# Kernel tuning notes

Hardware: AMD Instinct MI355X
Metric: run time of the kernel (lower is better)

The kernel has to match this reference:

```python
import jax, jax.numpy as jnp
import numpy as np

COUPLE_STRENGTH = 0.1
ITER_FISTA = 16
ITER_EIGENVAL = 20


def setup_inputs() -> dict:
    key = jax.random.key(0)
    k1, k2 = jax.random.split(key)
    # light field patches: (b, N, u, v, s, t, ch)
    x = jax.random.normal(k1, (8, 256, 5, 5, 4, 4, 3), dtype=jnp.float32)
    dim_signal = 5 * 5 * 4 * 4 * 3  # 1200
    dim_dict = 2 * dim_signal       # overcompleteness = 2 -> 2400
    D = jax.random.normal(k2, (dim_signal, dim_dict), dtype=jnp.float32)
    D = D / jnp.linalg.norm(D, axis=0, keepdims=True)  # UnitNorm(axis=0) constraint
    return {"x": x, "dictionary": D}


def _max_eigval(D):
    """von Mises power iteration for largest eigenvalue of D^T D."""
    v0 = jax.random.normal(jax.random.key(42), (D.shape[1],), dtype=D.dtype)
    v0 = v0 / jnp.linalg.norm(v0)

    def step(v, _):
        w = D.T @ (D @ v)
        n = jnp.linalg.norm(w)
        return w / n, n

    _, norms = jax.lax.scan(step, v0, None, length=ITER_EIGENVAL)
    return norms[-1]


def _soft_threshold(x, thr):
    return jnp.sign(x) * jnp.maximum(jnp.abs(x) - thr, 0.0)


def _sparse_code_fista(x2, D):
    """x2: (B, N, dim_signal); D: (dim_signal, dim_dict) -> codes (B, N, dim_dict)."""
    L = _max_eigval(D)            # Lipschitz constant of grad of 0.5*||Dz - x||^2
    thr = COUPLE_STRENGTH / L
    z0 = jnp.zeros(x2.shape[:-1] + (D.shape[1],), dtype=x2.dtype)
    carry0 = (z0, z0, jnp.float32(1.0))  # (z, y, t)

    def step(carry, _):
        z, y, t = carry
        recon = jnp.einsum('bnk,dk->bnd', y, D)             # (B,N,ds)
        grad = jnp.einsum('bnd,dk->bnk', recon - x2, D)     # (B,N,dd)
        z_new = _soft_threshold(y - grad / L, thr)
        t_new = 0.5 * (1.0 + jnp.sqrt(1.0 + 4.0 * t * t))
        y_new = z_new + ((t - 1.0) / t_new) * (z_new - z)   # Nesterov momentum
        return (z_new, y_new, t_new), None

    (z, _, _), _ = jax.lax.scan(step, carry0, None, length=ITER_FISTA)
    return z


def reference(x, dictionary):
    B, N, u, v, s, t, ch = x.shape
    x2 = x.reshape(B, N, u * v * s * t * ch)
    code = jax.lax.stop_gradient(_sparse_code_fista(x2, dictionary))
    recon = jnp.einsum('bnk,dk->bnd', code, dictionary)  # matmul(x, D, transpose_b=True)
    return recon.reshape(B, N, u, v, s, t, ch)
```

## Files before the change

kernel.cpp:

```cpp
#include <hip/hip_runtime.h>
#include <hip/hip_bf16.h>
#include <cmath>

#define DS 1200
#define DD 2400
#define MR 2048
#define KP 1216
#define NP1 1280
#define NG 2432
#define PPI 150

typedef __attribute__((ext_vector_type(8))) short s16x8;
typedef __attribute__((ext_vector_type(4))) float f32x4;

__device__ __forceinline__ float s2f(short s) {
    union { unsigned u; float f; } c;
    c.u = ((unsigned)(unsigned short)s) << 16;
    return c.f;
}
__device__ __forceinline__ short f2s(float f) {
    __hip_bfloat16 h = __float2bfloat16(f);
    return *reinterpret_cast<short*>(&h);
}


__device__ __forceinline__ unsigned rotl32(unsigned x, int d) {
    return (x << d) | (x >> (32 - d));
}

__device__ void threefry2x32(unsigned k0, unsigned k1, unsigned x0, unsigned x1,
                             unsigned* o0, unsigned* o1) {
    unsigned ks0 = k0, ks1 = k1, ks2 = k0 ^ k1 ^ 0x1BD11BDAu;
    const int rotA[4] = {13, 15, 26, 6};
    const int rotB[4] = {17, 29, 16, 24};
    x0 += ks0; x1 += ks1;
    #pragma unroll
    for (int r = 0; r < 4; r++) { x0 += x1; x1 = rotl32(x1, rotA[r]); x1 ^= x0; }
    x0 += ks1; x1 += ks2 + 1u;
    #pragma unroll
    for (int r = 0; r < 4; r++) { x0 += x1; x1 = rotl32(x1, rotB[r]); x1 ^= x0; }
    x0 += ks2; x1 += ks0 + 2u;
    #pragma unroll
    for (int r = 0; r < 4; r++) { x0 += x1; x1 = rotl32(x1, rotA[r]); x1 ^= x0; }
    x0 += ks0; x1 += ks1 + 3u;
    #pragma unroll
    for (int r = 0; r < 4; r++) { x0 += x1; x1 = rotl32(x1, rotB[r]); x1 ^= x0; }
    x0 += ks1; x1 += ks2 + 4u;
    #pragma unroll
    for (int r = 0; r < 4; r++) { x0 += x1; x1 = rotl32(x1, rotA[r]); x1 ^= x0; }
    x0 += ks2; x1 += ks0 + 5u;
    *o0 = x0; *o1 = x1;
}

__device__ float erfinv_f32(float x) {
    float w = -logf((1.0f - x) * (1.0f + x));
    float p;
    if (w < 5.0f) {
        w -= 2.5f;
        p = 2.81022636e-08f;
        p = fmaf(p, w, 3.43273939e-07f);
        p = fmaf(p, w, -3.5233877e-06f);
        p = fmaf(p, w, -4.39150654e-06f);
        p = fmaf(p, w, 0.00021858087f);
        p = fmaf(p, w, -0.00125372503f);
        p = fmaf(p, w, -0.00417768164f);
        p = fmaf(p, w, 0.246640727f);
        p = fmaf(p, w, 1.50140941f);
    } else {
        w = sqrtf(w) - 3.0f;
        p = -0.000200214257f;
        p = fmaf(p, w, 0.000100950558f);
        p = fmaf(p, w, 0.00134934322f);
        p = fmaf(p, w, -0.00367342844f);
        p = fmaf(p, w, 0.00573950773f);
        p = fmaf(p, w, -0.0076224613f);
        p = fmaf(p, w, 0.00943887047f);
        p = fmaf(p, w, 1.00167406f);
        p = fmaf(p, w, 2.83297682f);
    }
    return p * x;
}

__device__ float bits_to_normal(unsigned bits) {
    unsigned fb = (bits >> 9) | 0x3F800000u;
    float u01 = __uint_as_float(fb) - 1.0f;
    const float lo = -0.99999994f;
    float u = u01 * 2.0f + lo;
    u = fmaxf(lo, u);
    return 1.41421356237f * erfinv_f32(u);
}

__global__ void k_init(float* __restrict__ w0, float* __restrict__ w1,
                       float* __restrict__ part) {
    int tid = threadIdx.x;
    for (int i = tid; i < 21 * PPI; i += 256) part[i] = 0.0f;
    if (tid < 32) {
        w0[2400 + tid] = 0.0f;
        w1[2400 + tid] = 0.0f;
    }
    __shared__ float red[256];
    float local2 = 0.0f;
    for (int p = tid; p < DS; p += 256) {
        unsigned r0, r1;
        threefry2x32(0u, 42u, (unsigned)p, (unsigned)(DS + p), &r0, &r1);
        float n0 = bits_to_normal(r0);
        float n1 = bits_to_normal(r1);
        w0[p] = n0;
        w0[DS + p] = n1;
        local2 += n0 * n0 + n1 * n1;
    }
    red[tid] = local2;
    __syncthreads();
    for (int s = 128; s > 0; s >>= 1) {
        if (tid < s) red[tid] += red[tid + s];
        __syncthreads();
    }
    if (tid == 0) part[0] = red[0];
}

__global__ __launch_bounds__(1024) void k_gmv(const short* __restrict__ Grm,
                                              const float* __restrict__ win,
                                              const float* __restrict__ partin,
                                              float* __restrict__ wout,
                                              float* __restrict__ partout) {
    float s2 = 0.0f;
    for (int i = 0; i < PPI; i++) s2 += partin[i];
    float rn = 1.0f / sqrtf(s2);
    int wave = threadIdx.x >> 6, lane = threadIdx.x & 63;
    int row = blockIdx.x * 16 + wave;
    const s16x8* gh = (const s16x8*)(Grm + (size_t)row * NG);
    const float4* w4 = (const float4*)win;
    float acc = 0.0f;
    #pragma unroll
    for (int i = 0; i < 5; i++) {
        int c = lane + i * 64;
        if (c < 304) {
            s16x8 h = gh[c];
            float4 wa = w4[c * 2], wb = w4[c * 2 + 1];
            acc += s2f(h[0]) * wa.x + s2f(h[1]) * wa.y;
            acc += s2f(h[2]) * wa.z + s2f(h[3]) * wa.w;
            acc += s2f(h[4]) * wb.x + s2f(h[5]) * wb.y;
            acc += s2f(h[6]) * wb.z + s2f(h[7]) * wb.w;
        }
    }
    #pragma unroll
    for (int off = 32; off > 0; off >>= 1) acc += __shfl_xor(acc, off, 64);
    __shared__ float red[16];
    if (lane == 0) {
        float val = acc * rn;
        wout[row] = val;
        red[wave] = val * val;
    }
    __syncthreads();
    if (threadIdx.x == 0) {
        float s = 0.0f;
        #pragma unroll
        for (int i = 0; i < 16; i++) s += red[i];
        partout[blockIdx.x] = s;
    }
}

__global__ void k_fin(const float* __restrict__ part20, float* __restrict__ scal) {
    if (threadIdx.x == 0) {
        float s = 0.0f;
        for (int i = 0; i < PPI; i++) s += part20[i];
        float L = sqrtf(s);
        scal[0] = L;
        scal[1] = 1.0f / L;
        scal[2] = 0.1f / L;
    }
}

__global__ void k_makeD(const float* __restrict__ D, short* __restrict__ Dp) {
    int p = blockIdx.x * 256 + threadIdx.x;
    if (p >= NP1 * NG) return;
    int tile = p >> 10, win = p & 1023;
    int row = win >> 3, e = win & 7;
    int mt = tile / (NG >> 3), ct = tile % (NG >> 3);
    int d = mt * 128 + row, n = ct * 8 + e;
    float v = (d < DS && n < DD) ? D[(size_t)d * DD + n] : 0.0f;
    Dp[p] = f2s(v);
}

__global__ void k_makeX(const float* __restrict__ x,
                        short* __restrict__ Xhi, short* __restrict__ Xlo) {
    int p = blockIdx.x * 256 + threadIdx.x;
    if (p >= MR * KP) return;
    int tile = p >> 10, win = p & 1023;
    int row = win >> 3, e = win & 7;
    int mt = tile / (KP >> 3), ct = tile % (KP >> 3);
    int m = mt * 128 + row, k = ct * 8 + e;
    float v = (k < DS) ? x[(size_t)m * DS + k] : 0.0f;
    short h = f2s(v);
    Xhi[p] = h;
    Xlo[p] = f2s(v - s2f(h));
}

__global__ void k_makeDt(const float* __restrict__ D,
                         short* __restrict__ Dthi, short* __restrict__ Dtlo) {
    __shared__ float t[32][33];
    int bc = blockIdx.x * 32;
    int bk = blockIdx.y * 32;
    int tx = threadIdx.x & 31, ty = threadIdx.x >> 5;
    for (int i = ty; i < 32; i += 8) {
        int k = bk + i, c = bc + tx;
        t[i][tx] = (k < DS && c < DD) ? D[(size_t)k * DD + c] : 0.0f;
    }
    __syncthreads();
    for (int i = ty; i < 32; i += 8) {
        int c = bc + i, k = bk + tx;
        float v = t[tx][i];
        short h = f2s(v);
        size_t po = ((size_t)(c >> 7) * (KP >> 3) + (k >> 3)) * 1024 +
                    ((c & 127) << 3) + (k & 7);
        Dthi[po] = h;
        Dtlo[po] = f2s(v - s2f(h));
    }
}

__global__ void k_makeW(const float* __restrict__ Gf, const float* __restrict__ scal,
                        short* __restrict__ Wp) {
    int i = blockIdx.x * 256 + threadIdx.x;
    if (i >= NG * NG / 8) return;
    float invL = scal[1];
    int e0 = i * 8;
    int band = e0 / (128 * NG);
    int rem = e0 - band * (128 * NG);
    int tile = rem >> 10;
    int row = (rem & 1023) >> 3;
    int m = band * 128 + row;
    int k0 = tile * 8;
    const float4* gp = (const float4*)(Gf + (size_t)m * NG + k0);
    float4 g0 = gp[0], g1 = gp[1];
    float gv[8] = {g0.x, g0.y, g0.z, g0.w, g1.x, g1.y, g1.z, g1.w};
    s16x8 wv;
    #pragma unroll
    for (int e = 0; e < 8; e++) {
        float wf = ((k0 + e == m) ? 1.0f : 0.0f) - gv[e] * invL;
        wv[e] = f2s(wf);
    }
    ((s16x8*)Wp)[i] = wv;
}

__global__ void k_fista0(const float* __restrict__ XD, const float* __restrict__ scal,
                         short* __restrict__ Z, short* __restrict__ Y) {
    int i = blockIdx.x * 256 + threadIdx.x;
    if (i >= MR * NG / 8) return;
    float invL = scal[1], thr = scal[2];
    int e0 = i * 8;
    int band = e0 / (128 * NG);
    int rem = e0 - band * (128 * NG);
    int tile = rem >> 10;
    int row = (rem & 1023) >> 3;
    int m = band * 128 + row;
    int n = tile * 8;
    const float4* xp = (const float4*)(XD + (size_t)m * NG + n);
    float4 v0 = xp[0], v1 = xp[1];
    float vs[8] = {v0.x, v0.y, v0.z, v0.w, v1.x, v1.y, v1.z, v1.w};
    s16x8 zs;
    #pragma unroll
    for (int k = 0; k < 8; k++) {
        float gs = vs[k] * invL;
        float az = fabsf(gs) - thr;
        float zn = (az > 0.0f) ? copysignf(az, gs) : 0.0f;
        zs[k] = f2s(zn);
    }
    ((s16x8*)Z)[i] = zs;
    ((s16x8*)Y)[i] = zs;
}

__device__ __forceinline__ void gload16(const void* g, void* l) {
    __builtin_amdgcn_global_load_lds(
        (const __attribute__((address_space(1))) unsigned int*)g,
        (__attribute__((address_space(3))) unsigned int*)l, 16, 0, 0);
}

template <int EPI, bool SPLIT>
__global__ __launch_bounds__(256, 4) void mfma_gemm(
    const short* __restrict__ Ah, const short* __restrict__ Al, int CA,
    const short* __restrict__ Bh, const short* __restrict__ Bl, int CB,
    int K, int swz,
    const float* __restrict__ XDc, const float* __restrict__ scal, float mom,
    short* __restrict__ Ynew, short* __restrict__ Zst,
    short* __restrict__ Grm,
    float* __restrict__ Out) {
    constexpr int ALO = 2048;
    constexpr int BHO = 4096;
    constexpr int BLO = 8192;
    constexpr int BUF = 12288;
    __shared__ __align__(16) short lds[2 * BUF];

    const int tid = threadIdx.x;
    const int w = tid >> 6, lane = tid & 63;
    const int fm = lane & 15, kg = lane >> 4;
    const int wr = w >> 1, wc = w & 1;

    int bx, by;
    if (swz) {
        int q = gridDim.x >> 3;
        int s = (blockIdx.x & 7) * q + (blockIdx.x >> 3);
        by = s & 31; bx = s >> 5;
    } else { bx = blockIdx.x; by = blockIdx.y; }
    const int m0 = by * 64, n0 = bx * 128;

    f32x4 acc[2][4];
    #pragma unroll
    for (int g = 0; g < 2; ++g)
        #pragma unroll
        for (int h = 0; h < 4; ++h) acc[g][h] = f32x4{0.f, 0.f, 0.f, 0.f};

    float invL = 0.0f, thr = 0.0f;
    if (EPI == 2) { invL = scal[1]; thr = scal[2]; }

    const int half = (m0 >> 6) & 1;
    const int nk = K / (SPLIT ? 32 : 64);

    const size_t AbS = (size_t)(m0 & ~127) * CA + w * 1024 + half * 512 + lane * 8;
    const size_t BbS = (size_t)n0 * CB + w * 512 + lane * 8;
    const size_t AbN = (size_t)(m0 & ~127) * CA + half * 512 + lane * 8;
    const size_t BbN = (size_t)n0 * CB + lane * 8;

    auto STAGE = [&](int t, int cur) {
        short* bp = &lds[cur * BUF];
        if constexpr (SPLIT) {
            const size_t kk = (size_t)t << 12;
            gload16(Ah + AbS + kk, bp + w * 512);
            gload16(Bh + BbS + kk, bp + BHO + w * 512);
            gload16(Bh + BbS + kk + 2048, bp + BHO + 2048 + w * 512);
            gload16(Al + AbS + kk, bp + ALO + w * 512);
            gload16(Bl + BbS + kk, bp + BLO + w * 512);
            gload16(Bl + BbS + kk + 2048, bp + BLO + 2048 + w * 512);
        } else {
            const size_t kk = (size_t)t << 13;
            const int cs0 = 2 * w, cs1 = 2 * w + 1;
            gload16(Ah + AbN + kk + cs0 * 1024, bp + cs0 * 512);
            gload16(Ah + AbN + kk + cs1 * 1024, bp + cs1 * 512);
            gload16(Bh + BbN + kk + cs0 * 1024,       bp + BHO + cs0 * 1024);
            gload16(Bh + BbN + kk + cs0 * 1024 + 512, bp + BHO + cs0 * 1024 + 512);
            gload16(Bh + BbN + kk + cs1 * 1024,       bp + BHO + cs1 * 1024);
            gload16(Bh + BbN + kk + cs1 * 1024 + 512, bp + BHO + cs1 * 1024 + 512);
        }
    };

    STAGE(0, 0);

    for (int t = 0; t < nk; ++t) {
        __syncthreads();
        if (t + 1 < nk) STAGE(t + 1, (t + 1) & 1);
        const short* bs = &lds[(t & 1) * BUF];

        #pragma unroll
        for (int ks = 0; ks < (SPLIT ? 1 : 2); ++ks) {
            const int c = ks * 4 + kg;
            s16x8 a[2], b[4];
            #pragma unroll
            for (int g = 0; g < 2; ++g)
                a[g] = *(const s16x8*)&bs[c * 512 + (wr * 32 + g * 16 + fm) * 8];
            #pragma unroll
            for (int h = 0; h < 4; ++h)
                b[h] = *(const s16x8*)&bs[BHO + c * 1024 + (wc * 64 + h * 16 + fm) * 8];
            if constexpr (SPLIT) {
                s16x8 a2[2], b2[4];
                #pragma unroll
                for (int g = 0; g < 2; ++g)
                    a2[g] = *(const s16x8*)&bs[ALO + c * 512 + (wr * 32 + g * 16 + fm) * 8];
                #pragma unroll
                for (int h = 0; h < 4; ++h)
                    b2[h] = *(const s16x8*)&bs[BLO + c * 1024 + (wc * 64 + h * 16 + fm) * 8];
                #pragma unroll
                for (int g = 0; g < 2; ++g)
                    #pragma unroll
                    for (int h = 0; h < 4; ++h) {
                        acc[g][h] = __builtin_amdgcn_mfma_f32_16x16x32_bf16(a[g], b[h], acc[g][h], 0, 0, 0);
                        acc[g][h] = __builtin_amdgcn_mfma_f32_16x16x32_bf16(a[g], b2[h], acc[g][h], 0, 0, 0);
                        acc[g][h] = __builtin_amdgcn_mfma_f32_16x16x32_bf16(a2[g], b[h], acc[g][h], 0, 0, 0);
                    }
            } else {
                #pragma unroll
                for (int g = 0; g < 2; ++g)
                    #pragma unroll
                    for (int h = 0; h < 4; ++h)
                        acc[g][h] = __builtin_amdgcn_mfma_f32_16x16x32_bf16(a[g], b[h], acc[g][h], 0, 0, 0);
            }
        }
    }

    #pragma unroll
    for (int g = 0; g < 2; ++g) {
        #pragma unroll
        for (int h = 0; h < 4; ++h) {
            #pragma unroll
            for (int j = 0; j < 4; ++j) {
                int m = m0 + wr * 32 + g * 16 + kg * 4 + j;
                int n = n0 + wc * 64 + h * 16 + fm;
                float v = acc[g][h][j];
                if (EPI == 0) {
                    if (n < DS) Out[(size_t)m * DS + n] = v;
                } else if (EPI == 2) {
                    size_t o = (size_t)m * NG + n;
                    size_t pz = (size_t)(m & ~127) * NG + ((n >> 3) << 10) +
                                ((m & 127) << 3) + (n & 7);
                    float gs = fmaf(XDc[o], invL, v);
                    float az = fabsf(gs) - thr;
                    float zn = (az > 0.0f) ? copysignf(az, gs) : 0.0f;
                    float zold = s2f(Zst[pz]);
                    float yn = zn + mom * (zn - zold);
                    Zst[pz] = f2s(zn);
                    Ynew[pz] = f2s(yn);
                } else if (EPI == 3) {
                    Out[(size_t)m * NG + n] = v;
                } else {
                    size_t o = (size_t)m * NG + n;
                    Grm[o] = f2s(v);
                    Out[o] = v;
                }
            }
        }
    }
}

extern "C" void kernel_launch(void* const* d_in, const int* in_sizes, int n_in,
                              void* d_out, int out_size, void* d_ws, size_t ws_size,
                              hipStream_t stream) {
    const float* x = (const float*)d_in[0];
    const float* D = (const float*)d_in[1];
    float* out = (float*)d_out;

    char* wsb = (char*)d_ws;
    float* w0 = (float*)wsb;
    float* w1 = w0 + 2432;
    float* part = w1 + 2432;
    float* scal = part + 3200;

    char* p = wsb + 65536;
    short* Dp   = (short*)p; p += (size_t)NP1 * NG * 2;
    short* Dthi = (short*)p; p += (size_t)NG * KP * 2;
    short* Dtlo = (short*)p; p += (size_t)NG * KP * 2;
    short* Xhi  = (short*)p; p += (size_t)MR * KP * 2;
    short* Xlo  = (short*)p; p += (size_t)MR * KP * 2;
    short* Wp   = (short*)p; p += (size_t)NG * NG * 2;
    short* Grm  = (short*)p; p += (size_t)NG * NG * 2;
    float* XD   = (float*)p; p += (size_t)MR * NG * 4;
    short* Ya   = (short*)p; p += (size_t)MR * NG * 2;
    short* Yb   = (short*)p; p += (size_t)MR * NG * 2;
    short* Zp   = (short*)p; p += (size_t)MR * NG * 2;
    float* Gf   = (float*)Ya;

    k_makeD<<<(NP1 * NG + 255) / 256, 256, 0, stream>>>(D, Dp);
    k_makeDt<<<dim3(NG / 32, KP / 32), 256, 0, stream>>>(D, Dthi, Dtlo);
    k_makeX<<<(MR * KP + 255) / 256, 256, 0, stream>>>(x, Xhi, Xlo);

    mfma_gemm<4, true><<<dim3(NG / 128, NG / 64), 256, 0, stream>>>(
        Dthi, Dtlo, KP, Dthi, Dtlo, KP, KP, 0,
        nullptr, nullptr, 0.0f, nullptr, nullptr, Grm, Gf);

    k_init<<<1, 256, 0, stream>>>(w0, w1, part);
    for (int j = 0; j < 20; j++) {
        const float* win = (j & 1) ? w1 : w0;
        float* wout = (j & 1) ? w0 : w1;
        k_gmv<<<PPI, 1024, 0, stream>>>(Grm, win, part + j * PPI, wout,
                                        part + (j + 1) * PPI);
    }
    k_fin<<<1, 64, 0, stream>>>(part + 20 * PPI, scal);

    k_makeW<<<(NG * NG / 8 + 255) / 256, 256, 0, stream>>>(Gf, scal, Wp);

    mfma_gemm<3, true><<<dim3(608), 256, 0, stream>>>(
        Xhi, Xlo, KP, Dthi, Dtlo, KP, KP, 1,
        nullptr, nullptr, 0.0f, nullptr, nullptr, nullptr, XD);

    k_fista0<<<(MR * NG / 8 + 255) / 256, 256, 0, stream>>>(XD, scal, Zp, Ya);

    float t = 1.6180339887f;
    for (int i = 1; i < 16; i++) {
        float tn = 0.5f * (1.0f + sqrtf(1.0f + 4.0f * t * t));
        float mom = (t - 1.0f) / tn;
        t = tn;
        short* Yc = (i & 1) ? Ya : Yb;
        short* Yn = (i & 1) ? Yb : Ya;
        mfma_gemm<2, false><<<dim3(608), 256, 0, stream>>>(
            Yc, nullptr, NG, Wp, nullptr, NG, NG, 1,
            XD, scal, mom, Yn, Zp, nullptr, nullptr);
    }

    mfma_gemm<0, false><<<dim3(320), 256, 0, stream>>>(
        Zp, nullptr, NG, Dp, nullptr, NG, NG, 1,
        nullptr, nullptr, 0.0f, nullptr, nullptr, nullptr, out);
}
```

Before: 882.3 us.

## Triple-buffer GEMM LDS pipeline and store pre-scaled XD as packed bf16

The MFMA GEMM moves from a double-buffered LDS pipeline to a triple-buffered one. It prefetches two stages ahead and uses a partial vmcnt wait plus a raw barrier in place of a full __syncthreads, so more global loads stay in flight while MFMAs run. The x·D result is now pre-scaled by 1/L and stored as bf16 in the tiled layout used by Z/Y, which halves the traffic each FISTA iteration spends reading the epilogue XD term. The costs are more LDS per block (occupancy hint lowered from 4 to 2) and bf16 rounding of the XD term.

```diff
diff --git a/kernel.cpp b/kernel.cpp
--- a/kernel.cpp
+++ b/kernel.cpp
@@ -242,25 +242,16 @@
     ((s16x8*)Wp)[i] = wv;
 }
 
-__global__ void k_fista0(const float* __restrict__ XD, const float* __restrict__ scal,
+__global__ void k_fista0(const short* __restrict__ XDL, const float* __restrict__ scal,
                          short* __restrict__ Z, short* __restrict__ Y) {
     int i = blockIdx.x * 256 + threadIdx.x;
     if (i >= MR * NG / 8) return;
-    float invL = scal[1], thr = scal[2];
-    int e0 = i * 8;
-    int band = e0 / (128 * NG);
-    int rem = e0 - band * (128 * NG);
-    int tile = rem >> 10;
-    int row = (rem & 1023) >> 3;
-    int m = band * 128 + row;
-    int n = tile * 8;
-    const float4* xp = (const float4*)(XD + (size_t)m * NG + n);
-    float4 v0 = xp[0], v1 = xp[1];
-    float vs[8] = {v0.x, v0.y, v0.z, v0.w, v1.x, v1.y, v1.z, v1.w};
+    float thr = scal[2];
+    s16x8 xv = ((const s16x8*)XDL)[i];
     s16x8 zs;
     #pragma unroll
     for (int k = 0; k < 8; k++) {
-        float gs = vs[k] * invL;
+        float gs = s2f(xv[k]);
         float az = fabsf(gs) - thr;
         float zn = (az > 0.0f) ? copysignf(az, gs) : 0.0f;
         zs[k] = f2s(zn);
@@ -276,11 +267,11 @@
 }
 
 template <int EPI, bool SPLIT>
-__global__ __launch_bounds__(256, 4) void mfma_gemm(
+__global__ __launch_bounds__(256, 2) void mfma_gemm(
     const short* __restrict__ Ah, const short* __restrict__ Al, int CA,
     const short* __restrict__ Bh, const short* __restrict__ Bl, int CB,
     int K, int swz,
-    const float* __restrict__ XDc, const float* __restrict__ scal, float mom,
+    const short* __restrict__ XDLp, const float* __restrict__ scal, float mom,
     short* __restrict__ Ynew, short* __restrict__ Zst,
     short* __restrict__ Grm,
     float* __restrict__ Out) {
@@ -288,7 +279,7 @@
     constexpr int BHO = 4096;
     constexpr int BLO = 8192;
     constexpr int BUF = 12288;
-    __shared__ __align__(16) short lds[2 * BUF];
+    __shared__ __align__(16) short lds[3 * BUF];
 
     const int tid = threadIdx.x;
     const int w = tid >> 6, lane = tid & 63;
@@ -310,7 +301,8 @@
         for (int h = 0; h < 4; ++h) acc[g][h] = f32x4{0.f, 0.f, 0.f, 0.f};
 
     float invL = 0.0f, thr = 0.0f;
-    if (EPI == 2) { invL = scal[1]; thr = scal[2]; }
+    if (EPI == 2) thr = scal[2];
+    if (EPI == 3) invL = scal[1];
 
     const int half = (m0 >> 6) & 1;
     const int nk = K / (SPLIT ? 32 : 64);
@@ -343,11 +335,18 @@
     };
 
     STAGE(0, 0);
-
+    STAGE(1, 1);
+
+    int rb = 0, sb = 2;
     for (int t = 0; t < nk; ++t) {
-        __syncthreads();
-        if (t + 1 < nk) STAGE(t + 1, (t + 1) & 1);
-        const short* bs = &lds[(t & 1) * BUF];
+        if (t < nk - 1)
+            asm volatile("s_waitcnt vmcnt(6)" ::: "memory");
+        else
+            asm volatile("s_waitcnt vmcnt(0)" ::: "memory");
+        __builtin_amdgcn_s_barrier();
+        asm volatile("" ::: "memory");
+        if (t + 2 < nk) STAGE(t + 2, sb);
+        const short* bs = &lds[rb * BUF];
 
         #pragma unroll
         for (int ks = 0; ks < (SPLIT ? 1 : 2); ++ks) {
@@ -383,6 +382,8 @@
                         acc[g][h] = __builtin_amdgcn_mfma_f32_16x16x32_bf16(a[g], b[h], acc[g][h], 0, 0, 0);
             }
         }
+        rb = (rb == 2) ? 0 : rb + 1;
+        sb = (sb == 2) ? 0 : sb + 1;
     }
 
     #pragma unroll
@@ -397,10 +398,9 @@
                 if (EPI == 0) {
                     if (n < DS) Out[(size_t)m * DS + n] = v;
                 } else if (EPI == 2) {
-                    size_t o = (size_t)m * NG + n;
                     size_t pz = (size_t)(m & ~127) * NG + ((n >> 3) << 10) +
                                 ((m & 127) << 3) + (n & 7);
-                    float gs = fmaf(XDc[o], invL, v);
+                    float gs = v + s2f(XDLp[pz]);
                     float az = fabsf(gs) - thr;
                     float zn = (az > 0.0f) ? copysignf(az, gs) : 0.0f;
                     float zold = s2f(Zst[pz]);
@@ -408,7 +408,9 @@
                     Zst[pz] = f2s(zn);
                     Ynew[pz] = f2s(yn);
                 } else if (EPI == 3) {
-                    Out[(size_t)m * NG + n] = v;
+                    size_t pz = (size_t)(m & ~127) * NG + ((n >> 3) << 10) +
+                                ((m & 127) << 3) + (n & 7);
+                    Ynew[pz] = f2s(v * invL);
                 } else {
                     size_t o = (size_t)m * NG + n;
                     Grm[o] = f2s(v);
@@ -440,7 +442,7 @@
     short* Xlo  = (short*)p; p += (size_t)MR * KP * 2;
     short* Wp   = (short*)p; p += (size_t)NG * NG * 2;
     short* Grm  = (short*)p; p += (size_t)NG * NG * 2;
-    float* XD   = (float*)p; p += (size_t)MR * NG * 4;
+    short* XDLp = (short*)p; p += (size_t)MR * NG * 2;
     short* Ya   = (short*)p; p += (size_t)MR * NG * 2;
     short* Yb   = (short*)p; p += (size_t)MR * NG * 2;
     short* Zp   = (short*)p; p += (size_t)MR * NG * 2;
@@ -467,9 +469,9 @@
 
     mfma_gemm<3, true><<<dim3(608), 256, 0, stream>>>(
         Xhi, Xlo, KP, Dthi, Dtlo, KP, KP, 1,
-        nullptr, nullptr, 0.0f, nullptr, nullptr, nullptr, XD);
-
-    k_fista0<<<(MR * NG / 8 + 255) / 256, 256, 0, stream>>>(XD, scal, Zp, Ya);
+        nullptr, scal, 0.0f, XDLp, nullptr, nullptr, nullptr);
+
+    k_fista0<<<(MR * NG / 8 + 255) / 256, 256, 0, stream>>>(XDLp, scal, Zp, Ya);
 
     float t = 1.6180339887f;
     for (int i = 1; i < 16; i++) {
@@ -480,7 +482,7 @@
         short* Yn = (i & 1) ? Yb : Ya;
         mfma_gemm<2, false><<<dim3(608), 256, 0, stream>>>(
             Yc, nullptr, NG, Wp, nullptr, NG, NG, 1,
-            XD, scal, mom, Yn, Zp, nullptr, nullptr);
+            XDLp, scal, mom, Yn, Zp, nullptr, nullptr);
     }
 
     mfma_gemm<0, false><<<dim3(320), 256, 0, stream>>>(
```

Result: slower. 1.002 ms (+13.6%).
